# Performance work log

Measured on AMD Instinct MI355X. Metric: run time of the kernel, lower is better.

The kernel has to match this reference:

```python
import jax, jax.numpy as jnp
import numpy as np

B, D, F, H = 4096, 1024, 1024, 8


def setup_inputs() -> dict:
    key = jax.random.key(0)
    k1, k2, k3, k4 = jax.random.split(key, 4)
    inputs = jax.random.normal(k1, (B, D), dtype=jnp.float32)
    indices = jax.random.randint(k2, (B,), 0, H, dtype=jnp.int64)
    # lecun_normal-like scale for kernel; zeros bias per flax defaults, but use
    # small random bias so gradients are nontrivial
    kernel = jax.random.normal(k3, (H, D, F), dtype=jnp.float32) / np.sqrt(D)
    bias = jax.random.normal(k4, (H, F), dtype=jnp.float32) * 0.01
    return {"inputs": inputs, "indices": indices, "kernel": kernel, "bias": bias}


def reference(inputs, indices, kernel, bias):
    # Original: per-example gather of kernel[idx] ([D,F]) then x[idx] @ w + b.
    # Equivalent math, vectorized: compute all heads densely then select the
    # routed head per example (avoids materializing a [B,D,F] gathered tensor).
    y = jnp.einsum("bd,hdf->bhf", inputs, kernel) + bias[None, :, :]  # [B,H,F]
    return y[jnp.arange(inputs.shape[0]), indices]  # [B,F]
```

## Files before the change

### kernel.cpp

```cpp
#include <hip/hip_runtime.h>


typedef __attribute__((ext_vector_type(8))) short bf16x8;
typedef __attribute__((ext_vector_type(4))) float f32x4;

#define WAITV(N) asm volatile("s_waitcnt vmcnt(" #N ")" ::: "memory")

static __device__ __forceinline__ unsigned short f2bf(float f) {
  union { float f; unsigned int u; } c; c.f = f;
  unsigned int u = c.u;
  return (unsigned short)((u + 0x7fffu + ((u >> 16) & 1u)) >> 16);
}

static __device__ __forceinline__ void gload16(const void* g, void* s) {
  __builtin_amdgcn_global_load_lds(
      (const __attribute__((address_space(1))) void*)g,
      (__attribute__((address_space(3))) void*)s, 16, 0, 0);
}

__global__ __launch_bounds__(256) void k_prep(
    const float* __restrict__ W, const int* __restrict__ idx,
    unsigned short* __restrict__ Wt, int* __restrict__ cnt,
    int* __restrict__ base8, int* __restrict__ rows) {
  const int bid = blockIdx.x;
  const int t = threadIdx.x;

  if (bid >= 2048) {
    __shared__ int sc[256][8];
    int myi[16];
#pragma unroll
    for (int i = 0; i < 4; ++i) {
      const int4 v = *(const int4*)(idx + t * 16 + i * 4);
      myi[i * 4 + 0] = v.x; myi[i * 4 + 1] = v.y;
      myi[i * 4 + 2] = v.z; myi[i * 4 + 3] = v.w;
    }
    int c[8];
#pragma unroll
    for (int h = 0; h < 8; ++h) c[h] = 0;
#pragma unroll
    for (int e = 0; e < 16; ++e)
#pragma unroll
      for (int h = 0; h < 8; ++h) c[h] += (myi[e] == h) ? 1 : 0;

    int val[8];
#pragma unroll
    for (int h = 0; h < 8; ++h) { val[h] = c[h]; sc[t][h] = c[h]; }
    __syncthreads();
    for (int off = 1; off < 256; off <<= 1) {
      int nb[8];
#pragma unroll
      for (int h = 0; h < 8; ++h) nb[h] = (t >= off) ? sc[t - off][h] : 0;
      __syncthreads();
#pragma unroll
      for (int h = 0; h < 8; ++h) { val[h] += nb[h]; sc[t][h] = val[h]; }
      __syncthreads();
    }
    int tot[8], excl[8];
#pragma unroll
    for (int h = 0; h < 8; ++h) tot[h] = sc[255][h];
#pragma unroll
    for (int h = 0; h < 8; ++h) excl[h] = val[h] - c[h];
    int bases[9];
    bases[0] = 0;
#pragma unroll
    for (int h = 0; h < 7; ++h) bases[h + 1] = (bases[h] + tot[h] + 7) & ~7;
    bases[8] = bases[7] + tot[7];
#pragma unroll
    for (int h = 0; h < 8; ++h) {
      int pos = bases[h] + excl[h];
#pragma unroll
      for (int e = 0; e < 16; ++e) {
        if (myi[e] == h) { rows[pos] = t * 16 + e; ++pos; }
      }
    }
    if (t < 56) {
      const int hh = t >> 3, j = t & 7;
      const int pos = bases[hh] + tot[hh] + j;
      if (pos < bases[hh + 1]) rows[pos] = 0;
    }
    if (t < 128) {
      const int pos = bases[8] + t;
      if (pos < 4160) rows[pos] = 0;
    }
    if (t < 8) cnt[t] = tot[t];
    if (t == 0) {
#pragma unroll
      for (int h = 0; h < 9; ++h) base8[h] = bases[h];
    }
    return;
  }

  __shared__ unsigned short tile[64][68];
  const int h = bid >> 8;
  const int rem = bid & 255;
  const int d0 = (rem >> 4) << 6;
  const int f0 = (rem & 15) << 6;
  const int c4 = (t & 15) * 4;
  const int r0 = t >> 4;
#pragma unroll
  for (int i = 0; i < 4; ++i) {
    const int r = r0 + i * 16;
    const float4 v = *(const float4*)(W + (size_t)(h * 1024 + d0 + r) * 1024 + f0 + c4);
    tile[r][c4 + 0] = f2bf(v.x);
    tile[r][c4 + 1] = f2bf(v.y);
    tile[r][c4 + 2] = f2bf(v.z);
    tile[r][c4 + 3] = f2bf(v.w);
  }
  __syncthreads();
  const int chunk = c4 >> 3;
  const int half = (c4 >> 2) & 1;
#pragma unroll
  for (int i = 0; i < 4; ++i) {
    const int fr = r0 + i * 16;
    const int frow = f0 + fr;
    ushort4 o;
    o.x = tile[c4 + 0][fr];
    o.y = tile[c4 + 1][fr];
    o.z = tile[c4 + 2][fr];
    o.w = tile[c4 + 3][fr];
    const int cS = chunk ^ (frow & 7);
    *(ushort4*)((char*)Wt + (size_t)(h * 1024 + frow) * 2048 +
                (d0 << 1) + (cS << 4) + (half << 3)) = o;
  }
}

__global__ __launch_bounds__(256) void k_gather(
    const float* __restrict__ X, const int* __restrict__ rows,
    unsigned short* __restrict__ Ap) {
  const int slot = blockIdx.x;
  const int b = rows[slot];
  const int t = threadIdx.x;
  const float4 v = *(const float4*)(X + (size_t)b * 1024 + t * 4);
  ushort4 o;
  o.x = f2bf(v.x); o.y = f2bf(v.y); o.z = f2bf(v.z); o.w = f2bf(v.w);
  const int g = t >> 4;
  const int cS = ((t >> 1) & 7) ^ (slot & 7);
  *(ushort4*)((char*)Ap + (size_t)slot * 2048 + (g << 7) + (cS << 4) +
              ((t & 1) << 3)) = o;
}

__global__ __launch_bounds__(256) void k_gemm(
    const unsigned short* __restrict__ Ap, const unsigned short* __restrict__ Wt,
    const int* __restrict__ rows, const int* __restrict__ cnt,
    const int* __restrict__ base8,
    const float* __restrict__ bias, float* __restrict__ out) {
  __shared__ __align__(16) unsigned short As[2][128 * 64];
  __shared__ __align__(16) unsigned short Bs[2][128 * 64];

  const int blk = blockIdx.x;
  const int h = blk & 7;
  const int nt = (blk >> 3) & 7;
  const int mt = blk >> 6;

  const int cnt_h = cnt[h];
  const int basep = base8[h];
  const int m0 = mt * 128;
  if (m0 >= cnt_h) return;
  const int n0 = nt * 128;

  const int t = threadIdx.x;
  const int lane = t & 63;
  const int wave = t >> 6;
  const int wr = wave >> 1, wc = wave & 1;

  const int srow = t >> 3;
  const int scol = (t & 7) << 4;
  const char* aRow[4];
  const char* bRow[4];
#pragma unroll
  for (int r = 0; r < 4; ++r) {
    int ar = basep + m0 + r * 32 + srow;
    ar = ar < 4223 ? ar : 4223;
    aRow[r] = (const char*)Ap + (size_t)ar * 2048 + scol;
    bRow[r] = (const char*)Wt + (size_t)(h * 1024 + n0 + r * 32 + srow) * 2048 + scol;
  }

  f32x4 acc[4][4];
#pragma unroll
  for (int m = 0; m < 4; ++m)
#pragma unroll
    for (int n = 0; n < 4; ++n)
      acc[m][n] = (f32x4){0.f, 0.f, 0.f, 0.f};

  auto stage = [&](int s, int k0) {
#pragma unroll
    for (int r = 0; r < 4; ++r)
      gload16(aRow[r] + k0 * 2, (char*)(&As[s][0]) + r * 4096 + t * 16);
#pragma unroll
    for (int r = 0; r < 4; ++r)
      gload16(bRow[r] + k0 * 2, (char*)(&Bs[s][0]) + r * 4096 + t * 16);
  };

  const int swz = (lane & 7) << 4;
  const int ra = (wr * 64 + (lane & 15)) * 128;
  const int rb = (wc * 64 + (lane & 15)) * 128;
  const int kc = (lane >> 4) << 4;

  auto compute = [&](int s) {
    const char* ab = (const char*)(&As[s][0]);
    const char* bb = (const char*)(&Bs[s][0]);
#pragma unroll
    for (int ksub = 0; ksub < 2; ++ksub) {
      const int co = ((ksub * 64) + kc) ^ swz;
      bf16x8 af[4], bfr[4];
#pragma unroll
      for (int a = 0; a < 4; ++a)
        af[a] = *(const bf16x8*)(ab + ra + a * 2048 + co);
#pragma unroll
      for (int b = 0; b < 4; ++b)
        bfr[b] = *(const bf16x8*)(bb + rb + b * 2048 + co);
#pragma unroll
      for (int a = 0; a < 4; ++a)
#pragma unroll
        for (int b = 0; b < 4; ++b)
          acc[a][b] = __builtin_amdgcn_mfma_f32_16x16x32_bf16(af[a], bfr[b], acc[a][b], 0, 0, 0);
    }
  };

  stage(0, 0);
  stage(1, 64);

  for (int ts = 0; ts < 14; ++ts) {
    WAITV(8);
    __builtin_amdgcn_s_barrier();
    __builtin_amdgcn_sched_barrier(0);
    compute(ts & 1);
    __builtin_amdgcn_s_barrier();
    __builtin_amdgcn_sched_barrier(0);
    stage(ts & 1, (ts + 2) * 64);
    __builtin_amdgcn_sched_barrier(0);
  }
  WAITV(8);
  __builtin_amdgcn_s_barrier();
  __builtin_amdgcn_sched_barrier(0);
  compute(0);
  WAITV(0);
  __builtin_amdgcn_s_barrier();
  __builtin_amdgcn_sched_barrier(0);
  compute(1);

  int rmap[4][4];
  bool vld[4][4];
#pragma unroll
  for (int m = 0; m < 4; ++m) {
#pragma unroll
    for (int j = 0; j < 4; ++j) {
      const int lr = wr * 64 + m * 16 + (lane >> 4) * 4 + j;
      const bool v = (m0 + lr) < cnt_h;
      vld[m][j] = v;
      rmap[m][j] = v ? rows[basep + m0 + lr] : 0;
    }
  }
#pragma unroll
  for (int n = 0; n < 4; ++n) {
    const int c = n0 + wc * 64 + n * 16 + (lane & 15);
    const float bv = bias[h * 1024 + c];
#pragma unroll
    for (int m = 0; m < 4; ++m) {
#pragma unroll
      for (int j = 0; j < 4; ++j) {
        if (vld[m][j])
          out[(size_t)rmap[m][j] * 1024 + c] = acc[m][n][j] + bv;
      }
    }
  }
}

extern "C" void kernel_launch(void* const* d_in, const int* in_sizes, int n_in,
                              void* d_out, int out_size, void* d_ws, size_t ws_size,
                              hipStream_t stream) {
  const float* X = (const float*)d_in[0];
  const int* idx = (const int*)d_in[1];
  const float* W = (const float*)d_in[2];
  const float* bias = (const float*)d_in[3];
  float* out = (float*)d_out;

  char* ws = (char*)d_ws;
  int* cnt = (int*)ws;
  int* base8 = (int*)(ws + 64);
  int* rows = (int*)(ws + 256);
  unsigned short* Wt = (unsigned short*)(ws + 32768);
  unsigned short* Ap = (unsigned short*)(ws + 32768 + 16777216);

  k_prep<<<dim3(2049), 256, 0, stream>>>(W, idx, Wt, cnt, base8, rows);
  k_gather<<<dim3(4160), 256, 0, stream>>>(X, rows, Ap);
  k_gemm<<<dim3(8 * 8 * 32), 256, 0, stream>>>(Ap, Wt, rows, cnt, base8, bias, out);
}
```

Measured before the change: 55.17 us.

## Split GEMM K dimension in two with atomic accumulation and bias prefill

The per-head GEMM splits K into two halves with a 32-wide K step, doubling the number of work groups so more CUs are busy when each head has few rows. Partial sums are added into the output with unsafeAtomicAdd. The output is first filled with the routed bias inside the gather kernel. The XOR swizzle on the weight and activation staging layouts is dropped in favour of plain row-major layouts. Risks: more output traffic from atomics, possible LDS bank conflicts without the swizzle, removal of the row clamp on A loads, and only 16 M-tiles per head (2048 rows), which breaks if a head receives more rows.

New measurement: 66.42 us. 1.2x slower.

```diff
diff --git a/kernel.cpp b/kernel.cpp
--- a/kernel.cpp
+++ b/kernel.cpp
@@ -107,73 +107,66 @@
     tile[r][c4 + 3] = f2bf(v.w);
   }
   __syncthreads();
-  const int chunk = c4 >> 3;
-  const int half = (c4 >> 2) & 1;
 #pragma unroll
   for (int i = 0; i < 4; ++i) {
     const int fr = r0 + i * 16;
-    const int frow = f0 + fr;
     ushort4 o;
     o.x = tile[c4 + 0][fr];
     o.y = tile[c4 + 1][fr];
     o.z = tile[c4 + 2][fr];
     o.w = tile[c4 + 3][fr];
-    const int cS = chunk ^ (frow & 7);
-    *(ushort4*)((char*)Wt + (size_t)(h * 1024 + frow) * 2048 +
-                (d0 << 1) + (cS << 4) + (half << 3)) = o;
+    *(ushort4*)(Wt + (size_t)(h * 1024 + f0 + fr) * 1024 + d0 + c4) = o;
   }
 }
 
 __global__ __launch_bounds__(256) void k_gather(
-    const float* __restrict__ X, const int* __restrict__ rows,
-    unsigned short* __restrict__ Ap) {
+    const float* __restrict__ X, const int* __restrict__ idx,
+    const int* __restrict__ rows, unsigned short* __restrict__ Ap,
+    const float* __restrict__ bias, float* __restrict__ out) {
   const int slot = blockIdx.x;
   const int b = rows[slot];
   const int t = threadIdx.x;
   const float4 v = *(const float4*)(X + (size_t)b * 1024 + t * 4);
   ushort4 o;
   o.x = f2bf(v.x); o.y = f2bf(v.y); o.z = f2bf(v.z); o.w = f2bf(v.w);
-  const int g = t >> 4;
-  const int cS = ((t >> 1) & 7) ^ (slot & 7);
-  *(ushort4*)((char*)Ap + (size_t)slot * 2048 + (g << 7) + (cS << 4) +
-              ((t & 1) << 3)) = o;
+  *(ushort4*)(Ap + (size_t)slot * 1024 + t * 4) = o;
+  const int h = idx[b];
+  const float4 bv = *(const float4*)(bias + h * 1024 + t * 4);
+  *(float4*)(out + (size_t)b * 1024 + t * 4) = bv;
 }
 
 __global__ __launch_bounds__(256) void k_gemm(
     const unsigned short* __restrict__ Ap, const unsigned short* __restrict__ Wt,
     const int* __restrict__ rows, const int* __restrict__ cnt,
     const int* __restrict__ base8,
-    const float* __restrict__ bias, float* __restrict__ out) {
-  __shared__ __align__(16) unsigned short As[2][128 * 64];
-  __shared__ __align__(16) unsigned short Bs[2][128 * 64];
+    float* __restrict__ out) {
+  __shared__ __align__(16) unsigned short As[2][128 * 32];
+  __shared__ __align__(16) unsigned short Bs[2][128 * 32];
 
   const int blk = blockIdx.x;
   const int h = blk & 7;
   const int nt = (blk >> 3) & 7;
-  const int mt = blk >> 6;
+  const int ks = (blk >> 6) & 1;
+  const int mt = blk >> 7;
 
   const int cnt_h = cnt[h];
   const int basep = base8[h];
   const int m0 = mt * 128;
   if (m0 >= cnt_h) return;
   const int n0 = nt * 128;
+  const int kb = ks * 512;
 
   const int t = threadIdx.x;
   const int lane = t & 63;
   const int wave = t >> 6;
   const int wr = wave >> 1, wc = wave & 1;
 
-  const int srow = t >> 3;
-  const int scol = (t & 7) << 4;
-  const char* aRow[4];
-  const char* bRow[4];
-#pragma unroll
-  for (int r = 0; r < 4; ++r) {
-    int ar = basep + m0 + r * 32 + srow;
-    ar = ar < 4223 ? ar : 4223;
-    aRow[r] = (const char*)Ap + (size_t)ar * 2048 + scol;
-    bRow[r] = (const char*)Wt + (size_t)(h * 1024 + n0 + r * 32 + srow) * 2048 + scol;
-  }
+  const int srow = t >> 2;
+  const int schunk = (t & 3) << 4;
+  const char* aSrc0 = (const char*)Ap + (size_t)(basep + m0 + srow) * 2048 + schunk;
+  const char* aSrc1 = aSrc0 + (size_t)64 * 2048;
+  const char* bSrc0 = (const char*)Wt + (size_t)(h * 1024 + n0 + srow) * 2048 + schunk;
+  const char* bSrc1 = bSrc0 + (size_t)64 * 2048;
 
   f32x4 acc[4][4];
 #pragma unroll
@@ -183,54 +176,47 @@
       acc[m][n] = (f32x4){0.f, 0.f, 0.f, 0.f};
 
   auto stage = [&](int s, int k0) {
-#pragma unroll
-    for (int r = 0; r < 4; ++r)
-      gload16(aRow[r] + k0 * 2, (char*)(&As[s][0]) + r * 4096 + t * 16);
-#pragma unroll
-    for (int r = 0; r < 4; ++r)
-      gload16(bRow[r] + k0 * 2, (char*)(&Bs[s][0]) + r * 4096 + t * 16);
+    const int kby = k0 * 2;
+    gload16(aSrc0 + kby, (char*)(&As[s][0]) + t * 16);
+    gload16(aSrc1 + kby, (char*)(&As[s][0]) + 4096 + t * 16);
+    gload16(bSrc0 + kby, (char*)(&Bs[s][0]) + t * 16);
+    gload16(bSrc1 + kby, (char*)(&Bs[s][0]) + 4096 + t * 16);
   };
 
-  const int swz = (lane & 7) << 4;
-  const int ra = (wr * 64 + (lane & 15)) * 128;
-  const int rb = (wc * 64 + (lane & 15)) * 128;
-  const int kc = (lane >> 4) << 4;
+  const int ra = (wr * 64 + (lane & 15)) * 64 + (lane >> 4) * 16;
+  const int rb = (wc * 64 + (lane & 15)) * 64 + (lane >> 4) * 16;
 
   auto compute = [&](int s) {
     const char* ab = (const char*)(&As[s][0]);
     const char* bb = (const char*)(&Bs[s][0]);
-#pragma unroll
-    for (int ksub = 0; ksub < 2; ++ksub) {
-      const int co = ((ksub * 64) + kc) ^ swz;
-      bf16x8 af[4], bfr[4];
-#pragma unroll
-      for (int a = 0; a < 4; ++a)
-        af[a] = *(const bf16x8*)(ab + ra + a * 2048 + co);
-#pragma unroll
-      for (int b = 0; b < 4; ++b)
-        bfr[b] = *(const bf16x8*)(bb + rb + b * 2048 + co);
-#pragma unroll
-      for (int a = 0; a < 4; ++a)
-#pragma unroll
-        for (int b = 0; b < 4; ++b)
-          acc[a][b] = __builtin_amdgcn_mfma_f32_16x16x32_bf16(af[a], bfr[b], acc[a][b], 0, 0, 0);
-    }
+    bf16x8 af[4], bfr[4];
+#pragma unroll
+    for (int m = 0; m < 4; ++m)
+      af[m] = *(const bf16x8*)(ab + ra + m * 1024);
+#pragma unroll
+    for (int n = 0; n < 4; ++n)
+      bfr[n] = *(const bf16x8*)(bb + rb + n * 1024);
+#pragma unroll
+    for (int m = 0; m < 4; ++m)
+#pragma unroll
+      for (int n = 0; n < 4; ++n)
+        acc[m][n] = __builtin_amdgcn_mfma_f32_16x16x32_bf16(af[m], bfr[n], acc[m][n], 0, 0, 0);
   };
 
-  stage(0, 0);
-  stage(1, 64);
+  stage(0, kb);
+  stage(1, kb + 32);
 
   for (int ts = 0; ts < 14; ++ts) {
-    WAITV(8);
+    WAITV(4);
     __builtin_amdgcn_s_barrier();
     __builtin_amdgcn_sched_barrier(0);
     compute(ts & 1);
     __builtin_amdgcn_s_barrier();
     __builtin_amdgcn_sched_barrier(0);
-    stage(ts & 1, (ts + 2) * 64);
+    stage(ts & 1, kb + (ts + 2) * 32);
     __builtin_amdgcn_sched_barrier(0);
   }
-  WAITV(8);
+  WAITV(4);
   __builtin_amdgcn_s_barrier();
   __builtin_amdgcn_sched_barrier(0);
   compute(0);
@@ -254,13 +240,12 @@
 #pragma unroll
   for (int n = 0; n < 4; ++n) {
     const int c = n0 + wc * 64 + n * 16 + (lane & 15);
-    const float bv = bias[h * 1024 + c];
 #pragma unroll
     for (int m = 0; m < 4; ++m) {
 #pragma unroll
       for (int j = 0; j < 4; ++j) {
         if (vld[m][j])
-          out[(size_t)rmap[m][j] * 1024 + c] = acc[m][n][j] + bv;
+          unsafeAtomicAdd(&out[(size_t)rmap[m][j] * 1024 + c], acc[m][n][j]);
       }
     }
   }
@@ -283,6 +268,6 @@
   unsigned short* Ap = (unsigned short*)(ws + 32768 + 16777216);
 
   k_prep<<<dim3(2049), 256, 0, stream>>>(W, idx, Wt, cnt, base8, rows);
-  k_gather<<<dim3(4160), 256, 0, stream>>>(X, rows, Ap);
-  k_gemm<<<dim3(8 * 8 * 32), 256, 0, stream>>>(Ap, Wt, rows, cnt, base8, bias, out);
-}
+  k_gather<<<dim3(4160), 256, 0, stream>>>(X, idx, rows, Ap, bias, out);
+  k_gemm<<<dim3(8 * 8 * 2 * 16), 256, 0, stream>>>(Ap, Wt, rows, cnt, base8, out);
+}
```
